# Performance work log

Hardware: AMD Instinct MI355X
Metric: run time of the kernel (lower is better)

Reference implementation:

```python
import jax, jax.numpy as jnp
import numpy as np

N = 50000       # nodes
E = 800000      # edges (before self-loops)
F_IN = 128
HID = 64
HEADS = 4
OUT_DIM = 128
N_CLS = 2
NG = 500        # num graphs
SLOPE = 0.2     # GATConv leaky_relu negative slope
EPS = 1e-5      # BatchNorm eps


def setup_inputs() -> dict:
    key = jax.random.key(0)
    ks = jax.random.split(key, 24)
    s = 0.05
    d = {
        "x": jax.random.normal(ks[0], (N, F_IN), jnp.float32),
        "edge_index": jax.random.randint(ks[1], (2, E), 0, N, jnp.int64),
        "batch": jnp.sort(jax.random.randint(ks[2], (N,), 0, NG, jnp.int64)),
        # GATConv 1
        "W1": jax.random.normal(ks[3], (F_IN, HEADS * HID), jnp.float32) * s,
        "att_src1": jax.random.normal(ks[4], (HEADS, HID), jnp.float32) * s,
        "att_dst1": jax.random.normal(ks[5], (HEADS, HID), jnp.float32) * s,
        "b1": jnp.zeros((HEADS * HID,), jnp.float32),
        # BN1 (eval mode)
        "g1": jnp.ones((HEADS * HID,), jnp.float32),
        "be1": jnp.zeros((HEADS * HID,), jnp.float32),
        "rm1": jnp.zeros((HEADS * HID,), jnp.float32),
        "rv1": jnp.ones((HEADS * HID,), jnp.float32),
        # GATConv 2
        "W2": jax.random.normal(ks[6], (HEADS * HID, HEADS * HID), jnp.float32) * s,
        "att_src2": jax.random.normal(ks[7], (HEADS, HID), jnp.float32) * s,
        "att_dst2": jax.random.normal(ks[8], (HEADS, HID), jnp.float32) * s,
        "b2": jnp.zeros((HEADS * HID,), jnp.float32),
        # BN2 (eval mode)
        "g2": jnp.ones((HEADS * HID,), jnp.float32),
        "be2": jnp.zeros((HEADS * HID,), jnp.float32),
        "rm2": jnp.zeros((HEADS * HID,), jnp.float32),
        "rv2": jnp.ones((HEADS * HID,), jnp.float32),
        # MLP head
        "lw1": jax.random.normal(ks[9], (HEADS * HID, OUT_DIM), jnp.float32) * s,
        "lb1": jnp.zeros((OUT_DIM,), jnp.float32),
        "lw2": jax.random.normal(ks[10], (OUT_DIM, N_CLS), jnp.float32) * s,
        "lb2": jnp.zeros((N_CLS,), jnp.float32),
    }
    return d


def _gat_conv(x, src, dst, W, a_src, a_dst, b):
    """PyG GATConv (concat heads, add_self_loops=True, eval -> no dropout)."""
    n = x.shape[0]
    h = (x @ W).reshape(n, HEADS, -1)            # [N, H, C]
    loop = jnp.arange(n)
    s = jnp.concatenate([src, loop])             # self-loops appended
    d = jnp.concatenate([dst, loop])
    a_s = jnp.sum(h * a_src, axis=-1)            # [N, H]
    a_d = jnp.sum(h * a_dst, axis=-1)            # [N, H]
    e = jax.nn.leaky_relu(a_s[s] + a_d[d], SLOPE)   # [Et, H]
    # softmax over incoming edges per destination node
    m = jax.ops.segment_max(e, d, num_segments=n)
    ex = jnp.exp(e - m[d])
    denom = jax.ops.segment_sum(ex, d, num_segments=n)
    alpha = ex / denom[d]                        # [Et, H]
    msg = h[s] * alpha[:, :, None]               # [Et, H, C]
    out = jax.ops.segment_sum(msg, d, num_segments=n)
    return out.reshape(n, -1) + b


def _bn_eval(x, g, be, rm, rv):
    return (x - rm) * jax.lax.rsqrt(rv + EPS) * g + be


def reference(x, edge_index, batch, W1, att_src1, att_dst1, b1, g1, be1, rm1, rv1,
              W2, att_src2, att_dst2, b2, g2, be2, rm2, rv2, lw1, lb1, lw2, lb2):
    src, dst = edge_index[0], edge_index[1]
    h = jax.nn.relu(_gat_conv(x, src, dst, W1, att_src1, att_dst1, b1))
    h = _bn_eval(h, g1, be1, rm1, rv1)
    h = jax.nn.relu(_gat_conv(h, src, dst, W2, att_src2, att_dst2, b2))
    h = _bn_eval(h, g2, be2, rm2, rv2)
    # global mean pool over graphs
    sums = jax.ops.segment_sum(h, batch, num_segments=NG)
    cnt = jax.ops.segment_sum(jnp.ones((h.shape[0],), h.dtype), batch, num_segments=NG)
    pooled = sums / jnp.clip(cnt, 1.0)[:, None]
    z = jax.nn.relu(pooled @ lw1 + lb1)
    return z @ lw2 + lb2
```

## Files before the change

### kernel.cpp

```cpp
#include <hip/hip_runtime.h>
#include <hip/hip_bf16.h>
#include <math.h>

#define N_NODES 50000
#define M_PAD   50048
#define TILE_M  64
#define NBLK_GEMM (M_PAD / TILE_M)
#define NBLK_GEMM2 (M_PAD / 128)
#define N_EDGES 800000
#define EHALF   (N_EDGES / 2)
#define NBLK_BUILD ((EHALF + 255) / 256)
#define F_IN 128
#define HID 64
#define HEADS 4
#define FEAT 256
#define OUT_DIM 128
#define N_CLS 2
#define NG 500
#define SLOPE 0.2f
#define BN_EPS 1e-5f
#define ECAP 64

#define T_W1  (F_IN * 256)
#define T_W2  (FEAT * 256)
#define HPAD_ULL ((M_PAD - N_NODES) * FEAT / 4)
#define PREP_THREADS (T_W1 + T_W2 + HPAD_ULL + N_NODES)
#define NBLK_PREP ((PREP_THREADS + 255) / 256)

typedef __attribute__((ext_vector_type(8))) short short8;
typedef __attribute__((ext_vector_type(4))) float floatx4;
typedef __attribute__((ext_vector_type(2))) float floatx2;

__device__ inline unsigned short f2bf(float f) {
    unsigned int u = __float_as_uint(f);
    unsigned int lsb = (u >> 16) & 1u;
    return (unsigned short)((u + 0x7fffu + lsb) >> 16);
}

__global__ __launch_bounds__(256) void prep_small(
    const float* __restrict__ W1, const float* __restrict__ W2,
    unsigned short* __restrict__ W1T, unsigned short* __restrict__ W2T,
    unsigned short* __restrict__ h1bf,
    int* __restrict__ deg, int* __restrict__ ell, int* __restrict__ ovf_cnt) {
    int gid = blockIdx.x * 256 + threadIdx.x;
    if (gid < T_W1) {
        int k = gid >> 8, n = gid & 255;
        W1T[n * F_IN + k] = f2bf(W1[gid]);
        return;
    }
    int j = gid - T_W1;
    if (j < T_W2) {
        int k = j >> 8, n = j & 255;
        W2T[n * FEAT + k] = f2bf(W2[j]);
        return;
    }
    j -= T_W2;
    if (j < HPAD_ULL) {
        ((unsigned long long*)(h1bf + (size_t)N_NODES * FEAT))[j] = 0ULL;
        return;
    }
    j -= HPAD_ULL;
    if (j < N_NODES) {
        deg[j] = 1;
        ell[(size_t)j * ECAP] = j;
        if (j == 0) *ovf_cnt = 0;
    }
}

template<int K, bool AF32, int TM>
__device__ __forceinline__ void gemm_core(
    const void* __restrict__ Av, const unsigned short* __restrict__ BT,
    const float* __restrict__ att_src, const float* __restrict__ att_dst,
    unsigned char* __restrict__ h8, float* __restrict__ a_s,
    float* __restrict__ a_d, int bid, unsigned char* smem_raw) {
    constexpr int LS = 40;
    constexpr int C8 = 272;
    constexpr int MI = TM / 16;
    int t = threadIdx.x;
    unsigned short* As = (unsigned short*)smem_raw;
    unsigned short* Bs = As + TM * LS;
    unsigned char*  s8 = smem_raw;
    int lane = t & 63, w = t >> 6;
    int row0 = bid * TM;
    int mrow = lane & 15, quad = lane >> 4;

    floatx4 acc[MI][4] = {};

    int rA = t >> 2, cA = (t & 3) * 8;

    const unsigned short* Ab = (const unsigned short*)Av;
    const float* Af = (const float*)Av;

    for (int k0 = 0; k0 < K; k0 += 32) {
        #pragma unroll
        for (int j = 0; j < TM / 64; j++) {
            int r = rA + j * 64;
            if (AF32) {
                uint4 pk = make_uint4(0, 0, 0, 0);
                if (row0 + r < N_NODES) {
                    float4 f0 = *(const float4*)&Af[(long long)(row0 + r) * K + k0 + cA];
                    float4 f1 = *(const float4*)&Af[(long long)(row0 + r) * K + k0 + cA + 4];
                    pk.x = (unsigned)f2bf(f0.x) | ((unsigned)f2bf(f0.y) << 16);
                    pk.y = (unsigned)f2bf(f0.z) | ((unsigned)f2bf(f0.w) << 16);
                    pk.z = (unsigned)f2bf(f1.x) | ((unsigned)f2bf(f1.y) << 16);
                    pk.w = (unsigned)f2bf(f1.z) | ((unsigned)f2bf(f1.w) << 16);
                }
                *(uint4*)&As[r * LS + cA] = pk;
            } else {
                *(uint4*)&As[r * LS + cA] =
                    *(const uint4*)&Ab[(long long)(row0 + r) * K + k0 + cA];
            }
        }
        #pragma unroll
        for (int j = 0; j < 4; j++) {
            int r = rA + j * 64;
            *(uint4*)&Bs[r * LS + cA] = *(const uint4*)&BT[(long long)r * K + k0 + cA];
        }
        __syncthreads();
        short8 bf[4];
        #pragma unroll
        for (int ni = 0; ni < 4; ni++)
            bf[ni] = *(const short8*)&Bs[(w * 64 + ni * 16 + mrow) * LS + quad * 8];
        #pragma unroll
        for (int mi = 0; mi < MI; mi++) {
            short8 af = *(const short8*)&As[(mi * 16 + mrow) * LS + quad * 8];
            #pragma unroll
            for (int ni = 0; ni < 4; ni++)
                acc[mi][ni] = __builtin_amdgcn_mfma_f32_16x16x32_bf16(af, bf[ni],
                                                                      acc[mi][ni], 0, 0, 0);
        }
        __syncthreads();
    }

    float ats[4], atd[4];
    #pragma unroll
    for (int ni = 0; ni < 4; ni++) {
        ats[ni] = att_src[w * 64 + ni * 16 + mrow];
        atd[ni] = att_dst[w * 64 + ni * 16 + mrow];
    }
    #pragma unroll
    for (int mi = 0; mi < MI; mi++) {
        #pragma unroll
        for (int r = 0; r < 4; r++) {
            int row = row0 + mi * 16 + quad * 4 + r;
            float ps = 0.f, pd = 0.f;
            #pragma unroll
            for (int ni = 0; ni < 4; ni++) {
                float v = acc[mi][ni][r];
                ps += v * ats[ni];
                pd += v * atd[ni];
            }
            #pragma unroll
            for (int off = 1; off < 16; off <<= 1) {
                ps += __shfl_xor(ps, off);
                pd += __shfl_xor(pd, off);
            }
            if (mrow == 0 && row < N_NODES) {
                a_s[row * 4 + w] = ps;
                a_d[row * 4 + w] = pd;
            }
        }
    }

    #pragma unroll
    for (int mi = 0; mi < MI; mi++)
        #pragma unroll
        for (int r = 0; r < 4; r++) {
            int row = mi * 16 + quad * 4 + r;
            #pragma unroll
            for (int ni = 0; ni < 4; ni += 2) {
                int pk = __builtin_amdgcn_cvt_pk_fp8_f32(acc[mi][ni][r],
                                                         acc[mi][ni + 1][r], 0, false);
                s8[row * C8 + w * 64 + ni * 16 + mrow]       = (unsigned char)(pk & 0xff);
                s8[row * C8 + w * 64 + (ni + 1) * 16 + mrow] = (unsigned char)((pk >> 8) & 0xff);
            }
        }
    __syncthreads();
    if (TM == 64) {
        int r2 = t >> 2, q = t & 3;
        const uint4* sp = (const uint4*)&s8[r2 * C8 + q * 64];
        uint4* dp = (uint4*)&h8[(long long)(row0 + r2) * FEAT + q * 64];
        #pragma unroll
        for (int k = 0; k < 4; k++)
            dp[k] = sp[k];
    } else {
        int r2 = t >> 1, half = t & 1;
        const uint4* sp = (const uint4*)&s8[r2 * C8 + half * 128];
        uint4* dp = (uint4*)&h8[(long long)(row0 + r2) * FEAT + half * 128];
        #pragma unroll
        for (int k = 0; k < 8; k++)
            dp[k] = sp[k];
    }
}

__global__ __launch_bounds__(256, 4) void gemm1_build(
    const float* __restrict__ x, const unsigned short* __restrict__ BT,
    const float* __restrict__ att_src, const float* __restrict__ att_dst,
    unsigned char* __restrict__ h8, float* __restrict__ a_s,
    float* __restrict__ a_d,
    const int* __restrict__ src, const int* __restrict__ dst,
    int* __restrict__ deg, int* __restrict__ ell,
    int* __restrict__ ovf_cnt, int* __restrict__ ovf) {
    __shared__ __align__(16) unsigned char smem_raw[(TILE_M + FEAT) * 40 * 2];
    if (blockIdx.x >= NBLK_GEMM) {
        int i = (blockIdx.x - NBLK_GEMM) * 256 + threadIdx.x;
        if (i >= EHALF) return;
        int s0 = src[i],          d0 = dst[i];
        int s1 = src[i + EHALF],  d1 = dst[i + EHALF];
        int p0 = atomicAdd(&deg[d0], 1);
        int p1 = atomicAdd(&deg[d1], 1);
        if (p0 < ECAP) {
            ell[(size_t)d0 * ECAP + p0] = s0;
        } else {
            int k = atomicAdd(ovf_cnt, 1);
            ovf[2 * k] = s0; ovf[2 * k + 1] = d0;
        }
        if (p1 < ECAP) {
            ell[(size_t)d1 * ECAP + p1] = s1;
        } else {
            int k = atomicAdd(ovf_cnt, 1);
            ovf[2 * k] = s1; ovf[2 * k + 1] = d1;
        }
        return;
    }
    gemm_core<F_IN, true, TILE_M>(x, BT, att_src, att_dst, h8, a_s, a_d,
                                  blockIdx.x, smem_raw);
}

__global__ __launch_bounds__(256, 2) void gemm2k(
    const unsigned short* __restrict__ Ab, const unsigned short* __restrict__ BT,
    const float* __restrict__ att_src, const float* __restrict__ att_dst,
    unsigned char* __restrict__ h8, float* __restrict__ a_s,
    float* __restrict__ a_d) {
    __shared__ __align__(16) unsigned char smem_raw[128 * 272];
    gemm_core<FEAT, false, 128>(Ab, BT, att_src, att_dst, h8, a_s, a_d,
                                blockIdx.x, smem_raw);
}

__device__ __forceinline__ void gat_core(
    const int* __restrict__ deg_arr, const int* __restrict__ ell,
    const int* __restrict__ ovf_cnt, const int* __restrict__ ovf,
    const float* __restrict__ a_s, const float* __restrict__ a_d,
    const unsigned char* __restrict__ h8, const float* __restrict__ bias,
    const float* __restrict__ g, const float* __restrict__ be,
    const float* __restrict__ rm, const float* __restrict__ rv,
    unsigned short* __restrict__ out16) {
    int t = threadIdx.x;
    int lane = t & 63;
    int w = t >> 6;
    int hd = lane >> 4;
    int d = blockIdx.x * 4 + w;

    __shared__ float p_lds[4 * ECAP * 4];
    __shared__ int   o_lds[4 * ECAP];
    float* pw = &p_lds[w * ECAP * 4];
    int*   ow = &o_lds[w * ECAP];

    const unsigned int* __restrict__ H1 = (const unsigned int*)h8;

    int deg = deg_arr[d];
    float4 ad4 = *(const float4*)&a_d[d * 4];

    float den = 0.f;
    float4 acc = make_float4(0.f, 0.f, 0.f, 0.f);

    if (deg <= ECAP) {
        float lg[4] = {-INFINITY, -INFINITY, -INFINITY, -INFINITY};
        int s = 0;
        if (lane < deg) {
            s = ell[(size_t)d * ECAP + lane];
            float4 as4 = *(const float4*)&a_s[s * 4];
            float e0 = as4.x + ad4.x; lg[0] = e0 > 0.f ? e0 : SLOPE * e0;
            float e1 = as4.y + ad4.y; lg[1] = e1 > 0.f ? e1 : SLOPE * e1;
            float e2 = as4.z + ad4.z; lg[2] = e2 > 0.f ? e2 : SLOPE * e2;
            float e3 = as4.w + ad4.w; lg[3] = e3 > 0.f ? e3 : SLOPE * e3;
        }
        ow[lane] = s * 64;
        float mm = fmaxf(fmaxf(lg[0], lg[1]), fmaxf(lg[2], lg[3]));
        #pragma unroll
        for (int off = 1; off < 64; off <<= 1) mm = fmaxf(mm, __shfl_xor(mm, off));
        float4 pq = make_float4(0.f, 0.f, 0.f, 0.f);
        if (lane < deg) {
            pq.x = __expf(lg[0] - mm);
            pq.y = __expf(lg[1] - mm);
            pq.z = __expf(lg[2] - mm);
            pq.w = __expf(lg[3] - mm);
        }
        *(float4*)&pw[lane * 4] = pq;
        int deg4 = (deg + 3) & ~3;
        int cu[4];
        #pragma unroll
        for (int j = 0; j < 4; j++) cu[j] = (int)H1[ow[j] + lane];
        for (int e = 0; e < deg4; e += 4) {
            int nu[4] = {0, 0, 0, 0};
            if (e + 4 < deg4) {
                #pragma unroll
                for (int j = 0; j < 4; j++) nu[j] = (int)H1[ow[e + 4 + j] + lane];
            }
            #pragma unroll
            for (int j = 0; j < 4; j++) {
                float pj = pw[(e + j) * 4 + hd];
                den += pj;
                floatx2 lo = __builtin_amdgcn_cvt_pk_f32_fp8(cu[j], false);
                floatx2 hi = __builtin_amdgcn_cvt_pk_f32_fp8(cu[j], true);
                acc.x += pj * lo.x; acc.y += pj * lo.y;
                acc.z += pj * hi.x; acc.w += pj * hi.y;
            }
            #pragma unroll
            for (int j = 0; j < 4; j++) cu[j] = nu[j];
        }
    } else {
        float m_old;
        {
            int s = ell[(size_t)d * ECAP + lane];
            ow[lane] = s * 64;
            float4 as4 = *(const float4*)&a_s[s * 4];
            float lg[4];
            float e0 = as4.x + ad4.x; lg[0] = e0 > 0.f ? e0 : SLOPE * e0;
            float e1 = as4.y + ad4.y; lg[1] = e1 > 0.f ? e1 : SLOPE * e1;
            float e2 = as4.z + ad4.z; lg[2] = e2 > 0.f ? e2 : SLOPE * e2;
            float e3 = as4.w + ad4.w; lg[3] = e3 > 0.f ? e3 : SLOPE * e3;
            float mm = fmaxf(fmaxf(lg[0], lg[1]), fmaxf(lg[2], lg[3]));
            #pragma unroll
            for (int off = 1; off < 64; off <<= 1) mm = fmaxf(mm, __shfl_xor(mm, off));
            m_old = mm;
            float4 pq;
            pq.x = __expf(lg[0] - mm);
            pq.y = __expf(lg[1] - mm);
            pq.z = __expf(lg[2] - mm);
            pq.w = __expf(lg[3] - mm);
            *(float4*)&pw[lane * 4] = pq;
            for (int e = 0; e < ECAP; e++) {
                int oA = ow[e];
                float pA = pw[e * 4 + hd];
                int uA = (int)H1[oA + lane];
                den += pA;
                floatx2 a0 = __builtin_amdgcn_cvt_pk_f32_fp8(uA, false);
                floatx2 a1 = __builtin_amdgcn_cvt_pk_f32_fp8(uA, true);
                acc.x += pA * a0.x; acc.y += pA * a0.y;
                acc.z += pA * a1.x; acc.w += pA * a1.y;
            }
        }
        int nov = *ovf_cnt;
        for (int i = 0; i < nov; i++) {
            int s2 = ovf[2 * i], d2 = ovf[2 * i + 1];
            if (d2 != d) continue;
            float4 as4 = *(const float4*)&a_s[s2 * 4];
            float lg[4];
            float e0 = as4.x + ad4.x; lg[0] = e0 > 0.f ? e0 : SLOPE * e0;
            float e1 = as4.y + ad4.y; lg[1] = e1 > 0.f ? e1 : SLOPE * e1;
            float e2 = as4.z + ad4.z; lg[2] = e2 > 0.f ? e2 : SLOPE * e2;
            float e3 = as4.w + ad4.w; lg[3] = e3 > 0.f ? e3 : SLOPE * e3;
            float mmax = fmaxf(fmaxf(lg[0], lg[1]), fmaxf(lg[2], lg[3]));
            float m_new = fmaxf(m_old, mmax);
            float alpha = __expf(m_old - m_new);
            m_old = m_new;
            float ph = __expf(lg[hd] - m_new);
            acc.x *= alpha; acc.y *= alpha; acc.z *= alpha; acc.w *= alpha;
            den = den * alpha + ph;
            int u = (int)H1[s2 * 64 + lane];
            floatx2 a0 = __builtin_amdgcn_cvt_pk_f32_fp8(u, false);
            floatx2 a1 = __builtin_amdgcn_cvt_pk_f32_fp8(u, true);
            acc.x += ph * a0.x; acc.y += ph * a0.y;
            acc.z += ph * a1.x; acc.w += ph * a1.y;
        }
    }
    float inv = 1.f / den;
    int c0 = lane * 4;
    float4 bi = *(const float4*)&bias[c0];
    float4 gg = *(const float4*)&g[c0];
    float4 bb = *(const float4*)&be[c0];
    float4 mm4 = *(const float4*)&rm[c0];
    float4 vv = *(const float4*)&rv[c0];
    float v0 = fmaxf(acc.x * inv + bi.x, 0.f);
    float v1 = fmaxf(acc.y * inv + bi.y, 0.f);
    float v2 = fmaxf(acc.z * inv + bi.z, 0.f);
    float v3 = fmaxf(acc.w * inv + bi.w, 0.f);
    v0 = (v0 - mm4.x) * rsqrtf(vv.x + BN_EPS) * gg.x + bb.x;
    v1 = (v1 - mm4.y) * rsqrtf(vv.y + BN_EPS) * gg.y + bb.y;
    v2 = (v2 - mm4.z) * rsqrtf(vv.z + BN_EPS) * gg.z + bb.z;
    v3 = (v3 - mm4.w) * rsqrtf(vv.w + BN_EPS) * gg.w + bb.w;
    unsigned long long o =
        (unsigned long long)f2bf(v0) |
        ((unsigned long long)f2bf(v1) << 16) |
        ((unsigned long long)f2bf(v2) << 32) |
        ((unsigned long long)f2bf(v3) << 48);
    __builtin_nontemporal_store(o, (unsigned long long*)&out16[(long long)d * FEAT + c0]);
}

__global__ __launch_bounds__(256) void gat1(
    const int* __restrict__ deg_arr, const int* __restrict__ ell,
    const int* __restrict__ ovf_cnt, const int* __restrict__ ovf,
    const float* __restrict__ a_s, const float* __restrict__ a_d,
    const unsigned char* __restrict__ h8, const float* __restrict__ bias,
    const float* __restrict__ g, const float* __restrict__ be,
    const float* __restrict__ rm, const float* __restrict__ rv,
    unsigned short* __restrict__ out16) {
    gat_core(deg_arr, ell, ovf_cnt, ovf, a_s, a_d, h8, bias, g, be, rm, rv, out16);
}

__global__ __launch_bounds__(256) void gat2(
    const int* __restrict__ deg_arr, const int* __restrict__ ell,
    const int* __restrict__ ovf_cnt, const int* __restrict__ ovf,
    const float* __restrict__ a_s, const float* __restrict__ a_d,
    const unsigned char* __restrict__ h8, const float* __restrict__ bias,
    const float* __restrict__ g, const float* __restrict__ be,
    const float* __restrict__ rm, const float* __restrict__ rv,
    unsigned short* __restrict__ out16) {
    gat_core(deg_arr, ell, ovf_cnt, ovf, a_s, a_d, h8, bias, g, be, rm, rv, out16);
}

__global__ __launch_bounds__(256) void head_fused(
    const unsigned short* __restrict__ h2, const int* __restrict__ batch,
    const float* __restrict__ lw1, const float* __restrict__ lb1,
    const float* __restrict__ lw2, const float* __restrict__ lb2,
    float* __restrict__ out) {
    int gph = blockIdx.x;
    int t = threadIdx.x;
    __shared__ float pooled[FEAT];
    __shared__ float zl[OUT_DIM];
    __shared__ int lo_s, hi_s;
    if (t == 0) {
        int lo = 0, hi = N_NODES;
        while (lo < hi) { int mid = (lo + hi) >> 1; if (batch[mid] < gph) lo = mid + 1; else hi = mid; }
        lo_s = lo;
        int lo2 = 0, hi2 = N_NODES;
        while (lo2 < hi2) { int mid = (lo2 + hi2) >> 1; if (batch[mid] < gph + 1) lo2 = mid + 1; else hi2 = mid; }
        hi_s = lo2;
    }
    __syncthreads();
    int lo = lo_s, hi = hi_s;
    float a0 = 0.f, a1 = 0.f, a2 = 0.f, a3 = 0.f;
    int n = lo;
    for (; n + 3 < hi; n += 4) {
        a0 += __uint_as_float((unsigned)h2[(long long)n * FEAT + t] << 16);
        a1 += __uint_as_float((unsigned)h2[(long long)(n + 1) * FEAT + t] << 16);
        a2 += __uint_as_float((unsigned)h2[(long long)(n + 2) * FEAT + t] << 16);
        a3 += __uint_as_float((unsigned)h2[(long long)(n + 3) * FEAT + t] << 16);
    }
    for (; n < hi; n++) a0 += __uint_as_float((unsigned)h2[(long long)n * FEAT + t] << 16);
    float cnt = fmaxf((float)(hi - lo), 1.f);
    pooled[t] = (a0 + a1 + a2 + a3) / cnt;
    __syncthreads();
    int j = t >> 1, kh = t & 1;
    float zp = 0.f;
    #pragma unroll 8
    for (int k = kh * 128; k < kh * 128 + 128; k++)
        zp += pooled[k] * lw1[k * OUT_DIM + j];
    zp += __shfl_xor(zp, 1);
    if (kh == 0) zl[j] = fmaxf(zp + lb1[j], 0.f);
    __syncthreads();
    int w = t >> 6, lane = t & 63;
    if (w < 2) {
        float p = zl[lane] * lw2[lane * 2 + w] + zl[lane + 64] * lw2[(lane + 64) * 2 + w];
        #pragma unroll
        for (int off = 1; off < 64; off <<= 1) p += __shfl_xor(p, off);
        if (lane == 0) out[gph * 2 + w] = p + lb2[w];
    }
}

extern "C" void kernel_launch(void* const* d_in, const int* in_sizes, int n_in,
                              void* d_out, int out_size, void* d_ws, size_t ws_size,
                              hipStream_t stream) {
    const float* x       = (const float*)d_in[0];
    const int*   ei      = (const int*)d_in[1];
    const int*   batch   = (const int*)d_in[2];
    const float* W1      = (const float*)d_in[3];
    const float* att_s1  = (const float*)d_in[4];
    const float* att_d1  = (const float*)d_in[5];
    const float* b1      = (const float*)d_in[6];
    const float* g1      = (const float*)d_in[7];
    const float* be1     = (const float*)d_in[8];
    const float* rm1     = (const float*)d_in[9];
    const float* rv1     = (const float*)d_in[10];
    const float* W2      = (const float*)d_in[11];
    const float* att_s2  = (const float*)d_in[12];
    const float* att_d2  = (const float*)d_in[13];
    const float* b2      = (const float*)d_in[14];
    const float* g2      = (const float*)d_in[15];
    const float* be2     = (const float*)d_in[16];
    const float* rm2     = (const float*)d_in[17];
    const float* rv2     = (const float*)d_in[18];
    const float* lw1     = (const float*)d_in[19];
    const float* lb1     = (const float*)d_in[20];
    const float* lw2     = (const float*)d_in[21];
    const float* lb2     = (const float*)d_in[22];
    float* out           = (float*)d_out;

    const int* src = ei;
    const int* dst = ei + N_EDGES;

    char* p = (char*)d_ws;
    auto carve = [&p](size_t bytes) -> void* {
        void* r = (void*)p;
        p += (bytes + 63) & ~(size_t)63;
        return r;
    };
    unsigned short* h2bf = (unsigned short*)carve(sizeof(short) * (size_t)N_NODES * FEAT);
    float* a_s    = (float*)carve(sizeof(float) * N_NODES * HEADS);
    float* a_d    = (float*)carve(sizeof(float) * N_NODES * HEADS);
    int*   deg    = (int*)carve(sizeof(int) * N_NODES);
    int*   ovf_cnt= (int*)carve(sizeof(int) * 16);
    int*   ell    = (int*)carve(sizeof(int) * (size_t)N_NODES * ECAP);
    int*   ovf    = (int*)carve(sizeof(int) * 2 * (N_EDGES + N_NODES));
    unsigned char*  h8   = (unsigned char*)carve((size_t)M_PAD * FEAT);
    unsigned short* h1bf = (unsigned short*)carve(sizeof(short) * (size_t)M_PAD * FEAT);
    unsigned short* w1t  = (unsigned short*)carve(sizeof(short) * FEAT * F_IN);
    unsigned short* w2t  = (unsigned short*)carve(sizeof(short) * FEAT * FEAT);

    prep_small<<<NBLK_PREP, 256, 0, stream>>>(
        W1, W2, w1t, w2t, h1bf, deg, ell, ovf_cnt);

    gemm1_build<<<NBLK_GEMM + NBLK_BUILD, 256, 0, stream>>>(
        x, w1t, att_s1, att_d1, h8, a_s, a_d,
        src, dst, deg, ell, ovf_cnt, ovf);
    gat1<<<N_NODES / 4, 256, 0, stream>>>(deg, ell, ovf_cnt, ovf, a_s, a_d, h8,
                                          b1, g1, be1, rm1, rv1, h1bf);

    gemm2k<<<NBLK_GEMM2, 256, 0, stream>>>(
        h1bf, w2t, att_s2, att_d2, h8, a_s, a_d);
    gat2<<<N_NODES / 4, 256, 0, stream>>>(deg, ell, ovf_cnt, ovf, a_s, a_d, h8,
                                          b2, g2, be2, rm2, rv2, h2bf);

    head_fused<<<NG, 256, 0, stream>>>(h2bf, batch, lw1, lb1, lw2, lb2, out);
}
```

Before: 300.3 us.

## Fuse mean-pool into second GAT kernel and move W2 transpose into gemm1

The second GAT kernel now accumulates each block's four node outputs into per-graph fp32 pooled sums with atomics, using LDS to combine rows that share a graph id. This removes the bf16 h2 write and the head kernel's re-read of all node features, so the head only does the MLP on pooled values. The W2 bf16 transpose moves from prep_small into extra blocks of gemm1_build. Edge building now handles four edges per thread instead of two. The changes add a memset, a __syncthreads in the GAT epilogue, atomic contention on pooled, and a nondeterministic summation order.

```diff
diff --git a/kernel.cpp b/kernel.cpp
--- a/kernel.cpp
+++ b/kernel.cpp
@@ -8,8 +8,8 @@
 #define NBLK_GEMM (M_PAD / TILE_M)
 #define NBLK_GEMM2 (M_PAD / 128)
 #define N_EDGES 800000
-#define EHALF   (N_EDGES / 2)
-#define NBLK_BUILD ((EHALF + 255) / 256)
+#define EQ      (N_EDGES / 4)
+#define NBLK_BUILD ((EQ + 255) / 256)
 #define F_IN 128
 #define HID 64
 #define HEADS 4
@@ -23,8 +23,9 @@
 
 #define T_W1  (F_IN * 256)
 #define T_W2  (FEAT * 256)
+#define NBLK_W2T (T_W2 / 256)
 #define HPAD_ULL ((M_PAD - N_NODES) * FEAT / 4)
-#define PREP_THREADS (T_W1 + T_W2 + HPAD_ULL + N_NODES)
+#define PREP_THREADS (T_W1 + HPAD_ULL + N_NODES)
 #define NBLK_PREP ((PREP_THREADS + 255) / 256)
 
 typedef __attribute__((ext_vector_type(8))) short short8;
@@ -38,8 +39,7 @@
 }
 
 __global__ __launch_bounds__(256) void prep_small(
-    const float* __restrict__ W1, const float* __restrict__ W2,
-    unsigned short* __restrict__ W1T, unsigned short* __restrict__ W2T,
+    const float* __restrict__ W1, unsigned short* __restrict__ W1T,
     unsigned short* __restrict__ h1bf,
     int* __restrict__ deg, int* __restrict__ ell, int* __restrict__ ovf_cnt) {
     int gid = blockIdx.x * 256 + threadIdx.x;
@@ -49,12 +49,6 @@
         return;
     }
     int j = gid - T_W1;
-    if (j < T_W2) {
-        int k = j >> 8, n = j & 255;
-        W2T[n * FEAT + k] = f2bf(W2[j]);
-        return;
-    }
-    j -= T_W2;
     if (j < HPAD_ULL) {
         ((unsigned long long*)(h1bf + (size_t)N_NODES * FEAT))[j] = 0ULL;
         return;
@@ -195,6 +189,7 @@
 
 __global__ __launch_bounds__(256, 4) void gemm1_build(
     const float* __restrict__ x, const unsigned short* __restrict__ BT,
+    const float* __restrict__ W2, unsigned short* __restrict__ W2T,
     const float* __restrict__ att_src, const float* __restrict__ att_dst,
     unsigned char* __restrict__ h8, float* __restrict__ a_s,
     float* __restrict__ a_d,
@@ -202,29 +197,38 @@
     int* __restrict__ deg, int* __restrict__ ell,
     int* __restrict__ ovf_cnt, int* __restrict__ ovf) {
     __shared__ __align__(16) unsigned char smem_raw[(TILE_M + FEAT) * 40 * 2];
-    if (blockIdx.x >= NBLK_GEMM) {
-        int i = (blockIdx.x - NBLK_GEMM) * 256 + threadIdx.x;
-        if (i >= EHALF) return;
-        int s0 = src[i],          d0 = dst[i];
-        int s1 = src[i + EHALF],  d1 = dst[i + EHALF];
-        int p0 = atomicAdd(&deg[d0], 1);
-        int p1 = atomicAdd(&deg[d1], 1);
-        if (p0 < ECAP) {
-            ell[(size_t)d0 * ECAP + p0] = s0;
-        } else {
-            int k = atomicAdd(ovf_cnt, 1);
-            ovf[2 * k] = s0; ovf[2 * k + 1] = d0;
-        }
-        if (p1 < ECAP) {
-            ell[(size_t)d1 * ECAP + p1] = s1;
-        } else {
-            int k = atomicAdd(ovf_cnt, 1);
-            ovf[2 * k] = s1; ovf[2 * k + 1] = d1;
+    int bid = blockIdx.x;
+    if (bid >= NBLK_GEMM + NBLK_W2T) {
+        int i = (bid - NBLK_GEMM - NBLK_W2T) * 256 + threadIdx.x;
+        if (i >= EQ) return;
+        int ss[4], dd[4], pp[4];
+        #pragma unroll
+        for (int j = 0; j < 4; j++) {
+            ss[j] = src[i + j * EQ];
+            dd[j] = dst[i + j * EQ];
+        }
+        #pragma unroll
+        for (int j = 0; j < 4; j++)
+            pp[j] = atomicAdd(&deg[dd[j]], 1);
+        #pragma unroll
+        for (int j = 0; j < 4; j++) {
+            if (pp[j] < ECAP) {
+                ell[(size_t)dd[j] * ECAP + pp[j]] = ss[j];
+            } else {
+                int k = atomicAdd(ovf_cnt, 1);
+                ovf[2 * k] = ss[j]; ovf[2 * k + 1] = dd[j];
+            }
         }
         return;
     }
+    if (bid >= NBLK_GEMM) {
+        int j = (bid - NBLK_GEMM) * 256 + threadIdx.x;
+        int k = j >> 8, n = j & 255;
+        W2T[n * FEAT + k] = f2bf(W2[j]);
+        return;
+    }
     gemm_core<F_IN, true, TILE_M>(x, BT, att_src, att_dst, h8, a_s, a_d,
-                                  blockIdx.x, smem_raw);
+                                  bid, smem_raw);
 }
 
 __global__ __launch_bounds__(256, 2) void gemm2k(
@@ -237,6 +241,7 @@
                                 blockIdx.x, smem_raw);
 }
 
+template<bool POOL>
 __device__ __forceinline__ void gat_core(
     const int* __restrict__ deg_arr, const int* __restrict__ ell,
     const int* __restrict__ ovf_cnt, const int* __restrict__ ovf,
@@ -244,7 +249,8 @@
     const unsigned char* __restrict__ h8, const float* __restrict__ bias,
     const float* __restrict__ g, const float* __restrict__ be,
     const float* __restrict__ rm, const float* __restrict__ rv,
-    unsigned short* __restrict__ out16) {
+    unsigned short* __restrict__ out16,
+    const int* __restrict__ batch, float* __restrict__ pooled) {
     int t = threadIdx.x;
     int lane = t & 63;
     int w = t >> 6;
@@ -253,6 +259,8 @@
 
     __shared__ float p_lds[4 * ECAP * 4];
     __shared__ int   o_lds[4 * ECAP];
+    __shared__ float4 shv[4][64];
+    __shared__ int    shg[4];
     float* pw = &p_lds[w * ECAP * 4];
     int*   ow = &o_lds[w * ECAP];
 
@@ -380,12 +388,34 @@
     v1 = (v1 - mm4.y) * rsqrtf(vv.y + BN_EPS) * gg.y + bb.y;
     v2 = (v2 - mm4.z) * rsqrtf(vv.z + BN_EPS) * gg.z + bb.z;
     v3 = (v3 - mm4.w) * rsqrtf(vv.w + BN_EPS) * gg.w + bb.w;
-    unsigned long long o =
-        (unsigned long long)f2bf(v0) |
-        ((unsigned long long)f2bf(v1) << 16) |
-        ((unsigned long long)f2bf(v2) << 32) |
-        ((unsigned long long)f2bf(v3) << 48);
-    __builtin_nontemporal_store(o, (unsigned long long*)&out16[(long long)d * FEAT + c0]);
+    if (!POOL) {
+        unsigned long long o =
+            (unsigned long long)f2bf(v0) |
+            ((unsigned long long)f2bf(v1) << 16) |
+            ((unsigned long long)f2bf(v2) << 32) |
+            ((unsigned long long)f2bf(v3) << 48);
+        __builtin_nontemporal_store(o, (unsigned long long*)&out16[(long long)d * FEAT + c0]);
+    } else {
+        shv[w][lane] = make_float4(v0, v1, v2, v3);
+        if (lane == 0) shg[w] = (int)batch[d];
+        __syncthreads();
+        int cl = t >> 2, ce = t & 3;
+        float r0 = ((const float*)&shv[0][cl])[ce];
+        float r1 = ((const float*)&shv[1][cl])[ce];
+        float r2 = ((const float*)&shv[2][cl])[ce];
+        float r3 = ((const float*)&shv[3][cl])[ce];
+        int g0 = shg[0], g1 = shg[1], g2 = shg[2], g3 = shg[3];
+        if (g0 == g3) {
+            atomicAdd(&pooled[g0 * FEAT + t], r0 + r1 + r2 + r3);
+        } else {
+            float sum = r0;
+            int gp = g0;
+            if (g1 == gp) sum += r1; else { atomicAdd(&pooled[gp * FEAT + t], sum); gp = g1; sum = r1; }
+            if (g2 == gp) sum += r2; else { atomicAdd(&pooled[gp * FEAT + t], sum); gp = g2; sum = r2; }
+            if (g3 == gp) sum += r3; else { atomicAdd(&pooled[gp * FEAT + t], sum); gp = g3; sum = r3; }
+            atomicAdd(&pooled[gp * FEAT + t], sum);
+        }
+    }
 }
 
 __global__ __launch_bounds__(256) void gat1(
@@ -396,28 +426,30 @@
     const float* __restrict__ g, const float* __restrict__ be,
     const float* __restrict__ rm, const float* __restrict__ rv,
     unsigned short* __restrict__ out16) {
-    gat_core(deg_arr, ell, ovf_cnt, ovf, a_s, a_d, h8, bias, g, be, rm, rv, out16);
-}
-
-__global__ __launch_bounds__(256) void gat2(
+    gat_core<false>(deg_arr, ell, ovf_cnt, ovf, a_s, a_d, h8, bias, g, be,
+                    rm, rv, out16, nullptr, nullptr);
+}
+
+__global__ __launch_bounds__(256) void gat2_pool(
     const int* __restrict__ deg_arr, const int* __restrict__ ell,
     const int* __restrict__ ovf_cnt, const int* __restrict__ ovf,
     const float* __restrict__ a_s, const float* __restrict__ a_d,
     const unsigned char* __restrict__ h8, const float* __restrict__ bias,
     const float* __restrict__ g, const float* __restrict__ be,
     const float* __restrict__ rm, const float* __restrict__ rv,
-    unsigned short* __restrict__ out16) {
-    gat_core(deg_arr, ell, ovf_cnt, ovf, a_s, a_d, h8, bias, g, be, rm, rv, out16);
-}
-
-__global__ __launch_bounds__(256) void head_fused(
-    const unsigned short* __restrict__ h2, const int* __restrict__ batch,
+    const int* __restrict__ batch, float* __restrict__ pooled) {
+    gat_core<true>(deg_arr, ell, ovf_cnt, ovf, a_s, a_d, h8, bias, g, be,
+                   rm, rv, nullptr, batch, pooled);
+}
+
+__global__ __launch_bounds__(256) void head_mlp(
+    const float* __restrict__ pooled, const int* __restrict__ batch,
     const float* __restrict__ lw1, const float* __restrict__ lb1,
     const float* __restrict__ lw2, const float* __restrict__ lb2,
     float* __restrict__ out) {
     int gph = blockIdx.x;
     int t = threadIdx.x;
-    __shared__ float pooled[FEAT];
+    __shared__ float pl[FEAT];
     __shared__ float zl[OUT_DIM];
     __shared__ int lo_s, hi_s;
     if (t == 0) {
@@ -429,24 +461,14 @@
         hi_s = lo2;
     }
     __syncthreads();
-    int lo = lo_s, hi = hi_s;
-    float a0 = 0.f, a1 = 0.f, a2 = 0.f, a3 = 0.f;
-    int n = lo;
-    for (; n + 3 < hi; n += 4) {
-        a0 += __uint_as_float((unsigned)h2[(long long)n * FEAT + t] << 16);
-        a1 += __uint_as_float((unsigned)h2[(long long)(n + 1) * FEAT + t] << 16);
-        a2 += __uint_as_float((unsigned)h2[(long long)(n + 2) * FEAT + t] << 16);
-        a3 += __uint_as_float((unsigned)h2[(long long)(n + 3) * FEAT + t] << 16);
-    }
-    for (; n < hi; n++) a0 += __uint_as_float((unsigned)h2[(long long)n * FEAT + t] << 16);
-    float cnt = fmaxf((float)(hi - lo), 1.f);
-    pooled[t] = (a0 + a1 + a2 + a3) / cnt;
+    float cnt = fmaxf((float)(hi_s - lo_s), 1.f);
+    pl[t] = pooled[gph * FEAT + t] / cnt;
     __syncthreads();
     int j = t >> 1, kh = t & 1;
     float zp = 0.f;
     #pragma unroll 8
     for (int k = kh * 128; k < kh * 128 + 128; k++)
-        zp += pooled[k] * lw1[k * OUT_DIM + j];
+        zp += pl[k] * lw1[k * OUT_DIM + j];
     zp += __shfl_xor(zp, 1);
     if (kh == 0) zl[j] = fmaxf(zp + lb1[j], 0.f);
     __syncthreads();
@@ -496,7 +518,7 @@
         p += (bytes + 63) & ~(size_t)63;
         return r;
     };
-    unsigned short* h2bf = (unsigned short*)carve(sizeof(short) * (size_t)N_NODES * FEAT);
+    float* pooled = (float*)carve(sizeof(float) * NG * FEAT);
     float* a_s    = (float*)carve(sizeof(float) * N_NODES * HEADS);
     float* a_d    = (float*)carve(sizeof(float) * N_NODES * HEADS);
     int*   deg    = (int*)carve(sizeof(int) * N_NODES);
@@ -508,19 +530,21 @@
     unsigned short* w1t  = (unsigned short*)carve(sizeof(short) * FEAT * F_IN);
     unsigned short* w2t  = (unsigned short*)carve(sizeof(short) * FEAT * FEAT);
 
-    prep_small<<<NBLK_PREP, 256, 0, stream>>>(
-        W1, W2, w1t, w2t, h1bf, deg, ell, ovf_cnt);
-
-    gemm1_build<<<NBLK_GEMM + NBLK_BUILD, 256, 0, stream>>>(
-        x, w1t, att_s1, att_d1, h8, a_s, a_d,
+    hipMemsetAsync(pooled, 0, sizeof(float) * NG * FEAT, stream);
+
+    prep_small<<<NBLK_PREP, 256, 0, stream>>>(W1, w1t, h1bf, deg, ell, ovf_cnt);
+
+    gemm1_build<<<NBLK_GEMM + NBLK_W2T + NBLK_BUILD, 256, 0, stream>>>(
+        x, w1t, W2, w2t, att_s1, att_d1, h8, a_s, a_d,
         src, dst, deg, ell, ovf_cnt, ovf);
     gat1<<<N_NODES / 4, 256, 0, stream>>>(deg, ell, ovf_cnt, ovf, a_s, a_d, h8,
                                           b1, g1, be1, rm1, rv1, h1bf);
 
     gemm2k<<<NBLK_GEMM2, 256, 0, stream>>>(
         h1bf, w2t, att_s2, att_d2, h8, a_s, a_d);
-    gat2<<<N_NODES / 4, 256, 0, stream>>>(deg, ell, ovf_cnt, ovf, a_s, a_d, h8,
-                                          b2, g2, be2, rm2, rv2, h2bf);
-
-    head_fused<<<NG, 256, 0, stream>>>(h2bf, batch, lw1, lb1, lw2, lb2, out);
-}
+    gat2_pool<<<N_NODES / 4, 256, 0, stream>>>(deg, ell, ovf_cnt, ovf, a_s, a_d,
+                                               h8, b2, g2, be2, rm2, rv2,
+                                               batch, pooled);
+
+    head_mlp<<<NG, 256, 0, stream>>>(pooled, batch, lw1, lb1, lw2, lb2, out);
+}
```

Measured after the change: 286.5 us. 4.6% less time.
